# Kernel optimization log

Hardware: AMD Instinct MI355X
Metric: run time of the kernel (lower is better)

## Reference

```python
import jax, jax.numpy as jnp
import numpy as np

N, B, NPG, E = 16384, 64, 256, 524288
F_IN, POS_DIM, L_PE = 32, 3, 8
W, HEADS, LAYERS, DFF = 256, 8, 2, 1024
HID, OUT = 512, 64
S = NPG + 1
DH = W // HEADS


def _ln(x, s, b, eps=1e-5):
    m = jnp.mean(x, -1, keepdims=True)
    v = jnp.var(x, -1, keepdims=True)
    return (x - m) * jax.lax.rsqrt(v + eps) * s + b


def _gelu(x):
    # custom tanh-approx GELU from the source module
    c = float(np.sqrt(2.0 / np.pi))
    return 0.5 * x * (1.0 + jnp.tanh(c * (x + 0.044715 * x ** 3)))


def setup_inputs() -> dict:
    key = jax.random.key(0)
    ks = jax.random.split(key, 24)
    nrm = lambda k, shape, s=0.05: jax.random.normal(k, shape, jnp.float32) * s
    D_IN = F_IN + POS_DIM * L_PE  # 56
    inp = {}
    inp['x'] = jax.random.normal(ks[0], (N, F_IN), jnp.float32)
    inp['p'] = jax.random.uniform(ks[1], (N, POS_DIM), jnp.float32, -1.0, 1.0)
    inp['edge_index'] = jax.random.randint(ks[2], (2, E), 0, N, jnp.int32)
    inp['batch'] = (jnp.arange(N) // NPG).astype(jnp.int32)  # sorted, 64 equal graphs
    inp['gcn_w'] = nrm(ks[3], (D_IN, W), 0.1)
    inp['gcn_b'] = jnp.zeros((W,), jnp.float32)
    inp['cls_token'] = nrm(ks[4], (1, 1, W), 0.02)
    inp['ln_pre_s'] = jnp.ones((W,), jnp.float32)
    inp['ln_pre_b'] = jnp.zeros((W,), jnp.float32)
    inp['norm1_s'] = jnp.ones((LAYERS, W), jnp.float32)
    inp['norm1_b'] = jnp.zeros((LAYERS, W), jnp.float32)
    inp['in_proj_w'] = nrm(ks[5], (LAYERS, W, 3 * W))
    inp['in_proj_b'] = jnp.zeros((LAYERS, 3 * W), jnp.float32)
    inp['out_proj_w'] = nrm(ks[6], (LAYERS, W, W))
    inp['out_proj_b'] = jnp.zeros((LAYERS, W), jnp.float32)
    inp['norm2_s'] = jnp.ones((LAYERS, W), jnp.float32)
    inp['norm2_b'] = jnp.zeros((LAYERS, W), jnp.float32)
    inp['ff_w1'] = nrm(ks[7], (LAYERS, W, DFF))
    inp['ff_b1'] = jnp.zeros((LAYERS, DFF), jnp.float32)
    inp['ff_w2'] = nrm(ks[8], (LAYERS, DFF, W))
    inp['ff_b2'] = jnp.zeros((LAYERS, W), jnp.float32)
    inp['ln_post_s'] = jnp.ones((W,), jnp.float32)
    inp['ln_post_b'] = jnp.zeros((W,), jnp.float32)
    inp['dec_w1'] = nrm(ks[9], (W, HID))
    inp['dec_b1'] = jnp.zeros((HID,), jnp.float32)
    inp['dec_w2'] = nrm(ks[10], (HID, HID))
    inp['dec_b2'] = jnp.zeros((HID,), jnp.float32)
    inp['dec_w3'] = nrm(ks[11], (HID, OUT))
    inp['dec_b3'] = jnp.zeros((OUT,), jnp.float32)
    return inp


def _forward(x, p, gcn_w, gcn_b, cls_token, ln_pre_s, ln_pre_b, norm1_s, norm1_b,
             in_proj_w, in_proj_b, out_proj_w, out_proj_b, norm2_s, norm2_b,
             ff_w1, ff_b1, ff_w2, ff_b2, ln_post_s, ln_post_b,
             dec_w1, dec_b1, dec_w2, dec_b2, dec_w3, dec_b3, edge_index, batch):
    # positional encoding: sin(p * 2^i * pi), i = 0..L-1
    freqs = (2.0 ** jnp.arange(L_PE, dtype=jnp.float32)) * jnp.pi
    pe = jnp.sin(p[:, :, None] * freqs).reshape(N, POS_DIM * L_PE)
    xc = jnp.concatenate([x, pe], axis=-1)  # [N, 56]
    # GCNConv: x W, then sym-normalized aggregation with self loops, + bias
    xw = xc @ gcn_w  # [N, W]
    loop = jnp.arange(N, dtype=edge_index.dtype)
    row = jnp.concatenate([edge_index[0], loop])
    col = jnp.concatenate([edge_index[1], loop])
    deg = jax.ops.segment_sum(jnp.ones_like(row, dtype=xw.dtype), col, num_segments=N)
    dinv = jax.lax.rsqrt(jnp.maximum(deg, 1e-12))
    coef = dinv[row] * dinv[col]
    h = jax.ops.segment_sum(coef[:, None] * xw[row], col, num_segments=N) + gcn_b
    # to_dense_batch (batch is sorted graph ids)
    counts = jax.ops.segment_sum(jnp.ones((N,), jnp.int32), batch, num_segments=B)
    ptr = jnp.concatenate([jnp.zeros((1,), jnp.int32), jnp.cumsum(counts)[:-1]])
    pos = jnp.arange(N, dtype=jnp.int32) - ptr[batch]
    dense = jnp.zeros((B, NPG, W), h.dtype).at[batch, pos].set(h)
    mask = jnp.zeros((B, NPG), bool).at[batch, pos].set(True)
    # prepend cls token
    xd = jnp.concatenate([jnp.broadcast_to(cls_token, (B, 1, W)), dense], axis=1)  # [B,S,W]
    valid = jnp.concatenate([jnp.ones((B, 1), bool), mask], axis=1)  # [B,S]
    xd = _ln(xd, ln_pre_s, ln_pre_b)
    # causal mask with row 0 (cls) unmasked
    am = jnp.triu(jnp.ones((S, S), bool), k=1)
    am = am.at[0, :].set(False)
    allowed = (~am)[None, :, :] & valid[:, None, :]  # [B,S,S]
    scale = 1.0 / float(np.sqrt(DH))
    for l in range(LAYERS):
        h1 = _ln(xd, norm1_s[l], norm1_b[l])
        qkv = h1 @ in_proj_w[l] + in_proj_b[l]  # [B,S,3W]
        q, k, v = jnp.split(qkv, 3, axis=-1)
        q = q.reshape(B, S, HEADS, DH)
        k = k.reshape(B, S, HEADS, DH)
        v = v.reshape(B, S, HEADS, DH)
        sc = jnp.einsum('bqhd,bkhd->bhqk', q, k) * scale
        sc = jnp.where(allowed[:, None, :, :], sc, -1e9)
        a = jax.nn.softmax(sc, axis=-1)
        o = jnp.einsum('bhqk,bkhd->bqhd', a, v).reshape(B, S, W)
        xd = xd + (o @ out_proj_w[l] + out_proj_b[l])
        h2 = _ln(xd, norm2_s[l], norm2_b[l])
        # MLP(num_layers=2) applies activation after BOTH layers (incl. last)
        ff = _gelu(_gelu(h2 @ ff_w1[l] + ff_b1[l]) @ ff_w2[l] + ff_b2[l])
        xd = xd + ff
    cls = _ln(xd[:, 0, :], ln_post_s, ln_post_b)
    # decoder MLP(num_layers=3) with relu after every layer (incl. last)
    h3 = jax.nn.relu(cls @ dec_w1 + dec_b1)
    h3 = jax.nn.relu(h3 @ dec_w2 + dec_b2)
    return jax.nn.relu(h3 @ dec_w3 + dec_b3)


def reference(x, p, gcn_w, gcn_b, cls_token, ln_pre_s, ln_pre_b, norm1_s, norm1_b,
              in_proj_w, in_proj_b, out_proj_w, out_proj_b, norm2_s, norm2_b,
              ff_w1, ff_b1, ff_w2, ff_b2, ln_post_s, ln_post_b,
              dec_w1, dec_b1, dec_w2, dec_b2, dec_w3, dec_b3, edge_index, batch):
    return _forward(x, p, gcn_w, gcn_b, cls_token, ln_pre_s, ln_pre_b, norm1_s, norm1_b,
                    in_proj_w, in_proj_b, out_proj_w, out_proj_b, norm2_s, norm2_b,
                    ff_w1, ff_b1, ff_w2, ff_b2, ln_post_s, ln_post_b,
                    dec_w1, dec_b1, dec_w2, dec_b2, dec_w3, dec_b3, edge_index, batch)
```

## Files before the change

kernel.cpp:

```cpp
#include <hip/hip_runtime.h>
#include <math.h>

constexpr int N_NODES = 16384;
constexpr int BGRAPH  = 64;
constexpr int NEDGE   = 524288;
constexpr int SEQ     = 257;
constexpr int WDIM    = 256;
constexpr int DFF     = 1024;
constexpr int HID     = 512;
constexpr int MROWS   = BGRAPH * SEQ;

constexpr size_t F_Y    = 0;
constexpr size_t F_AGG  = F_Y    + (size_t)N_NODES * 64;
constexpr size_t F_XD   = F_AGG  + (size_t)N_NODES * 64;
constexpr size_t F_CLS  = F_XD   + (size_t)MROWS * WDIM;
constexpr size_t F_D1   = F_CLS  + (size_t)BGRAPH * WDIM;
constexpr size_t F_D2   = F_D1   + (size_t)BGRAPH * HID;
constexpr size_t F_WPAD = F_D2   + (size_t)BGRAPH * HID;
constexpr size_t F_DINV = F_WPAD + (size_t)64 * WDIM;
constexpr size_t F_XCLS = F_DINV + (size_t)N_NODES;
constexpr size_t F_IEND = F_XCLS + (size_t)BGRAPH * WDIM;

typedef __attribute__((ext_vector_type(8))) __bf16 bf16x8;
typedef __attribute__((ext_vector_type(4))) __bf16 bf16x4;
typedef __attribute__((ext_vector_type(4))) float f32x4;

__device__ __forceinline__ float gelu_f(float x) {
    float u = 0.7978845608028654f * (x + 0.044715f * x * x * x);
    return 0.5f * x * (1.0f + tanhf(u));
}

__global__ __launch_bounds__(256) void hist_kernel(const int* __restrict__ col, int* __restrict__ indeg) {
    int e = blockIdx.x * 256 + threadIdx.x;
    atomicAdd(&indeg[col[e]], 1);
}

__global__ __launch_bounds__(1024) void scan_kernel(const int* __restrict__ indeg, int* __restrict__ offs,
                                                    int* __restrict__ cursor, float* __restrict__ dinv) {
    __shared__ int parts[1024];
    int t = threadIdx.x;
    int base = t * 16;
    int loc[16];
    int s = 0;
#pragma unroll
    for (int i = 0; i < 16; ++i) { loc[i] = indeg[base + i]; s += loc[i]; }
    parts[t] = s;
    __syncthreads();
    for (int off = 1; off < 1024; off <<= 1) {
        int v = (t >= off) ? parts[t - off] : 0;
        __syncthreads();
        parts[t] += v;
        __syncthreads();
    }
    int run = (t == 0) ? 0 : parts[t - 1];
#pragma unroll
    for (int i = 0; i < 16; ++i) {
        offs[base + i] = run;
        cursor[base + i] = run;
        dinv[base + i] = rsqrtf((float)loc[i] + 1.0f);
        run += loc[i];
    }
    if (t == 1023) offs[N_NODES] = run;
}

__global__ __launch_bounds__(256) void fill_kernel(const int* __restrict__ ei, int* __restrict__ cursor,
                                                   int* __restrict__ csr) {
    int e = blockIdx.x * 256 + threadIdx.x;
    int r = ei[e];
    int c = ei[NEDGE + e];
    int pos = atomicAdd(&cursor[c], 1);
    csr[pos] = r;
}

__global__ __launch_bounds__(256) void y_kernel(const float* __restrict__ x, const float* __restrict__ p,
                                                const float* __restrict__ dinv, float* __restrict__ y) {
    int idx = blockIdx.x * 256 + threadIdx.x;
    int i = idx >> 6, d = idx & 63;
    float v = 0.f;
    if (d < 32) {
        v = x[i * 32 + d];
    } else if (d < 56) {
        int dd = d - 32;
        int dim = dd >> 3, j = dd & 7;
        v = sinf(p[i * 3 + dim] * (3.14159265358979323846f * (float)(1 << j)));
    }
    y[idx] = dinv[i] * v;
}

__global__ __launch_bounds__(256) void agg_kernel(const float* __restrict__ y, const float* __restrict__ dinv,
                                                  const int* __restrict__ offs, const int* __restrict__ csr,
                                                  float* __restrict__ agg) {
    int c = (blockIdx.x * 256 + threadIdx.x) >> 6;
    int lane = threadIdx.x & 63;
    float acc = y[(size_t)c * 64 + lane];
    int s = offs[c], e = offs[c + 1];
    for (int j = s; j < e; ++j) {
        int r = csr[j];
        acc += y[(size_t)r * 64 + lane];
    }
    agg[(size_t)c * 64 + lane] = dinv[c] * acc;
}

__global__ __launch_bounds__(256) void wpad_kernel(const float* __restrict__ w, float* __restrict__ wp) {
    int idx = blockIdx.x * 256 + threadIdx.x;
    wp[idx] = (idx < 56 * 256) ? w[idx] : 0.f;
}

__global__ __launch_bounds__(256) void cls_write(const float* __restrict__ tok, float* __restrict__ xd) {
    xd[(size_t)blockIdx.x * SEQ * WDIM + threadIdx.x] = tok[threadIdx.x];
}

template <int OUTBF>
__global__ __launch_bounds__(256) void ln4_kernel(const float* __restrict__ in, int rin_stride,
                                                  void* __restrict__ out,
                                                  const float* __restrict__ g, const float* __restrict__ be) {
    int w = threadIdx.x >> 6, lane = threadIdx.x & 63;
    int row = blockIdx.x * 4 + w;
    const float* ip = in + (size_t)row * rin_stride + lane * 4;
    f32x4 v = *(const f32x4*)ip;
    float s = v[0] + v[1] + v[2] + v[3];
    float ss = v[0] * v[0] + v[1] * v[1] + v[2] * v[2] + v[3] * v[3];
#pragma unroll
    for (int off = 1; off < 64; off <<= 1) { s += __shfl_xor(s, off); ss += __shfl_xor(ss, off); }
    float mean = s * 0.00390625f;
    float var = ss * 0.00390625f - mean * mean;
    float rs = rsqrtf(var + 1e-5f);
    f32x4 gv = *(const f32x4*)(g + lane * 4);
    f32x4 bv = *(const f32x4*)(be + lane * 4);
    if (OUTBF) {
        bf16x4 o;
#pragma unroll
        for (int i = 0; i < 4; ++i) o[i] = (__bf16)((v[i] - mean) * rs * gv[i] + bv[i]);
        *(bf16x4*)((__bf16*)out + (size_t)row * 256 + lane * 4) = o;
    } else {
        f32x4 o;
#pragma unroll
        for (int i = 0; i < 4; ++i) o[i] = (v[i] - mean) * rs * gv[i] + bv[i];
        *(f32x4*)((float*)out + (size_t)row * 256 + lane * 4) = o;
    }
}

__global__ __launch_bounds__(256) void tcast_kernel(const float* __restrict__ W, __bf16* __restrict__ Wt,
                                                    int K, int N) {
    __shared__ __bf16 T[64][65];
    int t = threadIdx.x;
    int k0 = blockIdx.x << 6, n0 = blockIdx.y << 6;
#pragma unroll
    for (int i = 0; i < 16; ++i) {
        int idx = t + i * 256;
        int k = idx >> 6, n = idx & 63;
        T[k][n] = (__bf16)W[(size_t)(k0 + k) * N + n0 + n];
    }
    __syncthreads();
#pragma unroll
    for (int i = 0; i < 16; ++i) {
        int idx = t + i * 256;
        int n = idx >> 6, k = idx & 63;
        Wt[(size_t)(n0 + n) * K + k0 + k] = T[k][n];
    }
}

constexpr int LP = 36;
template <int BN, int ACT, int OMODE>
__global__ __launch_bounds__(256) void gemm_bf(const __bf16* __restrict__ A, int lda,
                                               const __bf16* __restrict__ Bt,
                                               const float* __restrict__ bias,
                                               void* __restrict__ Cv, int ldc,
                                               int Ktot, int Mrows, int MBlocks, int NY) {
    constexpr int NTW = BN / 32;
    constexpr int AH = 128 * LP;
    constexpr int BH = BN * LP;
    __shared__ __bf16 As[2 * 128 * LP];
    __shared__ __bf16 Bs[2 * BN * LP];
    int f = blockIdx.x;
    int m8 = f & 7;
    int rest = f >> 3;
    int mg = rest / NY;
    int yb = rest - mg * NY;
    int mb = mg * 8 + m8;
    if (mb >= MBlocks) return;
    int m0 = mb << 7, n0 = yb * BN;

    int t = threadIdx.x;
    int w = t >> 6, L = t & 63;
    int wm = w >> 1, wn = w & 1;
    int lc = L & 15, quad = L >> 4;

    int sa_row = t >> 1, sa_off = (t & 1) << 4;
    const __bf16* ap = A + (size_t)(m0 + sa_row) * lda + sa_off;
    __bf16* as_dst = &As[sa_row * LP + sa_off];
    const __bf16* bp;
    __bf16* bs_dst;
    if constexpr (BN == 128) {
        bp = Bt + (size_t)(n0 + sa_row) * Ktot + sa_off;
        bs_dst = &Bs[sa_row * LP + sa_off];
    } else {
        int sb_row = t >> 2, sb_off = (t & 3) << 3;
        bp = Bt + (size_t)(n0 + sb_row) * Ktot + sb_off;
        bs_dst = &Bs[sb_row * LP + sb_off];
    }

    int a_base = (wm * 64 + lc) * LP + quad * 8;
    int b_base = (wn * (BN / 2) + lc) * LP + quad * 8;

    f32x4 acc[4][NTW] = {};

    bf16x8 ea0, ea1, eb0, eb1, oa0, oa1, ob0, ob1;
    ea0 = *(const bf16x8*)(ap);        ea1 = *(const bf16x8*)(ap + 8);
    oa0 = *(const bf16x8*)(ap + 32);   oa1 = *(const bf16x8*)(ap + 40);
    if constexpr (BN == 128) {
        eb0 = *(const bf16x8*)(bp);        eb1 = *(const bf16x8*)(bp + 8);
        ob0 = *(const bf16x8*)(bp + 32);   ob1 = *(const bf16x8*)(bp + 40);
    } else {
        eb0 = *(const bf16x8*)(bp);
        ob0 = *(const bf16x8*)(bp + 32);
    }

    for (int k0 = 0; k0 < Ktot; k0 += 64) {
        __syncthreads();
        *(bf16x8*)as_dst = ea0;
        *(bf16x8*)(as_dst + 8) = ea1;
        *(bf16x8*)(as_dst + AH) = oa0;
        *(bf16x8*)(as_dst + AH + 8) = oa1;
        if constexpr (BN == 128) {
            *(bf16x8*)bs_dst = eb0;
            *(bf16x8*)(bs_dst + 8) = eb1;
            *(bf16x8*)(bs_dst + BH) = ob0;
            *(bf16x8*)(bs_dst + BH + 8) = ob1;
        } else {
            *(bf16x8*)bs_dst = eb0;
            *(bf16x8*)(bs_dst + BH) = ob0;
        }
        __syncthreads();
        if (k0 + 64 < Ktot) {
            ea0 = *(const bf16x8*)(ap + k0 + 64);
            ea1 = *(const bf16x8*)(ap + k0 + 72);
            oa0 = *(const bf16x8*)(ap + k0 + 96);
            oa1 = *(const bf16x8*)(ap + k0 + 104);
            if constexpr (BN == 128) {
                eb0 = *(const bf16x8*)(bp + k0 + 64);
                eb1 = *(const bf16x8*)(bp + k0 + 72);
                ob0 = *(const bf16x8*)(bp + k0 + 96);
                ob1 = *(const bf16x8*)(bp + k0 + 104);
            } else {
                eb0 = *(const bf16x8*)(bp + k0 + 64);
                ob0 = *(const bf16x8*)(bp + k0 + 96);
            }
        }
        {
            bf16x8 af[4], bfr[NTW];
#pragma unroll
            for (int i = 0; i < 4; ++i) af[i] = *(const bf16x8*)&As[a_base + i * 16 * LP];
#pragma unroll
            for (int i = 0; i < NTW; ++i) bfr[i] = *(const bf16x8*)&Bs[b_base + i * 16 * LP];
#pragma unroll
            for (int mt = 0; mt < 4; ++mt)
#pragma unroll
                for (int nt = 0; nt < NTW; ++nt)
                    acc[mt][nt] = __builtin_amdgcn_mfma_f32_16x16x32_bf16(af[mt], bfr[nt], acc[mt][nt], 0, 0, 0);
        }
        {
            bf16x8 af[4], bfr[NTW];
#pragma unroll
            for (int i = 0; i < 4; ++i) af[i] = *(const bf16x8*)&As[AH + a_base + i * 16 * LP];
#pragma unroll
            for (int i = 0; i < NTW; ++i) bfr[i] = *(const bf16x8*)&Bs[BH + b_base + i * 16 * LP];
#pragma unroll
            for (int mt = 0; mt < 4; ++mt)
#pragma unroll
                for (int nt = 0; nt < NTW; ++nt)
                    acc[mt][nt] = __builtin_amdgcn_mfma_f32_16x16x32_bf16(af[mt], bfr[nt], acc[mt][nt], 0, 0, 0);
        }
    }

#pragma unroll
    for (int mt = 0; mt < 4; ++mt) {
        int gmb = m0 + wm * 64 + mt * 16 + quad * 4;
#pragma unroll
        for (int nt = 0; nt < NTW; ++nt) {
            int gn = n0 + wn * (BN / 2) + nt * 16 + lc;
            float bv = bias[gn];
#pragma unroll
            for (int r = 0; r < 4; ++r) {
                int gm = gmb + r;
                if (gm >= Mrows) continue;
                float v = acc[mt][nt][r] + bv;
                if (ACT == 1) v = gelu_f(v);
                if (OMODE == 0) {
                    ((__bf16*)Cv)[(size_t)gm * ldc + gn] = (__bf16)v;
                } else {
                    float* cp = (float*)Cv + (size_t)gm * ldc + gn;
                    *cp = v + *cp;
                }
            }
        }
    }
}

constexpr int PPITCH = 284;
__global__ __launch_bounds__(256, 2) void attn_mfma(const __bf16* __restrict__ qkvb,
                                                    __bf16* __restrict__ obuf) {
    __shared__ __bf16 Vt[32][PPITCH];
    __shared__ __bf16 Pb[4][16][PPITCH];
    int bb = blockIdx.x;
    int b = bb >> 3, h = bb & 7;
    int t = threadIdx.x;
    int w = t >> 6, L = t & 63;
    int c = L & 15, quad = L >> 4;
    const float scale = 0.17677669529663687f;
    const __bf16* qb = qkvb + (size_t)(b * SEQ) * 768 + h * 32;
    const __bf16* kb = qb + 256;
    const __bf16* vb = qb + 512;
    __bf16* ob = obuf + (size_t)(b * SEQ) * 256 + h * 32;

    for (int idx = t; idx < 272 * 4; idx += 256) {
        int key = idx >> 2, dc = (idx & 3) * 8;
        bf16x8 vv = {};
        if (key < SEQ) vv = *(const bf16x8*)(vb + (size_t)key * 768 + dc);
#pragma unroll
        for (int j = 0; j < 8; ++j) Vt[dc + j][key] = vv[j];
    }

    bf16x8 kfr[17];
#pragma unroll
    for (int tt = 0; tt < 17; ++tt) {
        int kr = tt * 16 + c; if (kr > 256) kr = 256;
        kfr[tt] = *(const bf16x8*)(kb + (size_t)kr * 768 + quad * 8);
    }
    __syncthreads();

#pragma unroll 1
    for (int qt = 0; qt < 5; ++qt) {
        int q0 = qt * 64 + w * 16;
        if (q0 > 256) continue;
        int ntiles = (qt == 0 && w == 0) ? 17 : (qt * 4 + w + 1);
        if (ntiles > 17) ntiles = 17;
        int nkc = (ntiles + 1) >> 1;

        bf16x8 qf;
        {
            int qr = q0 + c; if (qr > 256) qr = 256;
            qf = *(const bf16x8*)(qb + (size_t)qr * 768 + quad * 8);
        }

        f32x4 acc[17];
#pragma unroll
        for (int tt = 0; tt < 17; ++tt) {
            if (tt >= ntiles) continue;
            f32x4 z = {0.f, 0.f, 0.f, 0.f};
            acc[tt] = __builtin_amdgcn_mfma_f32_16x16x32_bf16(qf, kfr[tt], z, 0, 0, 0);
        }

        float inv[4];
#pragma unroll
        for (int j = 0; j < 4; ++j) {
            int q = q0 + quad * 4 + j;
            float mx = -3.0e38f;
#pragma unroll
            for (int tt = 0; tt < 17; ++tt) {
                if (tt >= ntiles) continue;
                int key = tt * 16 + c;
                bool ok = (key < SEQ) && (q == 0 || key <= q);
                float v = ok ? acc[tt][j] * scale : -3.0e38f;
                mx = fmaxf(mx, v);
            }
            mx = fmaxf(mx, __shfl_xor(mx, 1));
            mx = fmaxf(mx, __shfl_xor(mx, 2));
            mx = fmaxf(mx, __shfl_xor(mx, 4));
            mx = fmaxf(mx, __shfl_xor(mx, 8));
            float s = 0.f;
#pragma unroll
            for (int tt = 0; tt < 17; ++tt) {
                if (tt >= ntiles) continue;
                int key = tt * 16 + c;
                bool ok = (key < SEQ) && (q == 0 || key <= q);
                float pv = ok ? expf(acc[tt][j] * scale - mx) : 0.f;
                s += pv;
                Pb[w][quad * 4 + j][key] = (__bf16)pv;
            }
            if ((ntiles & 1) && ntiles < 17)
                Pb[w][quad * 4 + j][ntiles * 16 + c] = (__bf16)0.f;
            s += __shfl_xor(s, 1);
            s += __shfl_xor(s, 2);
            s += __shfl_xor(s, 4);
            s += __shfl_xor(s, 8);
            inv[j] = 1.0f / s;
        }

        f32x4 oacc0 = {0.f, 0.f, 0.f, 0.f};
        f32x4 oacc1 = {0.f, 0.f, 0.f, 0.f};
#pragma unroll
        for (int kc = 0; kc < 9; ++kc) {
            if (kc >= nkc) continue;
            int off = kc * 32 + quad * 8;
            bf16x8 af = {};
            bf16x8 bf0 = {};
            bf16x8 bf1 = {};
            if (off < 257) {
                af  = *(const bf16x8*)&Pb[w][c][off];
                bf0 = *(const bf16x8*)&Vt[c][off];
                bf1 = *(const bf16x8*)&Vt[16 + c][off];
            }
            oacc0 = __builtin_amdgcn_mfma_f32_16x16x32_bf16(af, bf0, oacc0, 0, 0, 0);
            oacc1 = __builtin_amdgcn_mfma_f32_16x16x32_bf16(af, bf1, oacc1, 0, 0, 0);
        }

#pragma unroll
        for (int j = 0; j < 4; ++j) {
            int q = q0 + quad * 4 + j;
            if (q < SEQ) {
                __bf16* op = ob + (size_t)q * 256;
                op[c]      = (__bf16)(oacc0[j] * inv[j]);
                op[16 + c] = (__bf16)(oacc1[j] * inv[j]);
            }
        }
    }
}

__global__ __launch_bounds__(256) void qcls_kernel(const __bf16* __restrict__ h1b,
                                                   const float* __restrict__ W,
                                                   const float* __restrict__ bias,
                                                   __bf16* __restrict__ qcls) {
    __shared__ float hrow[256];
    int b = blockIdx.x, t = threadIdx.x;
    hrow[t] = (float)h1b[(size_t)(b * SEQ) * 256 + t];
    __syncthreads();
    float s = bias[t];
    for (int k = 0; k < 256; ++k) s += hrow[k] * W[(size_t)k * 768 + t];
    qcls[b * 256 + t] = (__bf16)s;
}

__global__ __launch_bounds__(64) void attn_cls(const __bf16* __restrict__ qcls,
                                               const __bf16* __restrict__ qkvb,
                                               __bf16* __restrict__ ocls) {
    __shared__ float p[260];
    int bb = blockIdx.x;
    int b = bb >> 3, h = bb & 7;
    int lane = threadIdx.x;
    const float scale = 0.17677669529663687f;
    float q[32];
    const __bf16* qp = qcls + b * 256 + h * 32;
#pragma unroll
    for (int c = 0; c < 4; ++c) {
        bf16x8 v = *(const bf16x8*)(qp + c * 8);
#pragma unroll
        for (int e = 0; e < 8; ++e) q[c * 8 + e] = (float)v[e];
    }
    float sc[5];
    float mx = -3.0e38f;
#pragma unroll
    for (int i = 0; i < 5; ++i) {
        int j = lane + i * 64;
        float s = -3.0e38f;
        if (j < SEQ) {
            const __bf16* kp = qkvb + (size_t)(b * SEQ + j) * 768 + 256 + h * 32;
            float a = 0.f;
#pragma unroll
            for (int c = 0; c < 4; ++c) {
                bf16x8 v = *(const bf16x8*)(kp + c * 8);
#pragma unroll
                for (int e = 0; e < 8; ++e) a += q[c * 8 + e] * (float)v[e];
            }
            s = a * scale;
        }
        sc[i] = s;
        mx = fmaxf(mx, s);
    }
#pragma unroll
    for (int off = 1; off < 64; off <<= 1) mx = fmaxf(mx, __shfl_xor(mx, off));
    float sum = 0.f;
#pragma unroll
    for (int i = 0; i < 5; ++i) {
        int j = lane + i * 64;
        float e = (j < SEQ) ? expf(sc[i] - mx) : 0.f;
        sc[i] = e;
        sum += e;
    }
#pragma unroll
    for (int off = 1; off < 64; off <<= 1) sum += __shfl_xor(sum, off);
    float inv = 1.0f / sum;
#pragma unroll
    for (int i = 0; i < 5; ++i) {
        int j = lane + i * 64;
        if (j < SEQ) p[j] = sc[i] * inv;
    }
    __syncthreads();
    if (lane < 32) {
        float o = 0.f;
        for (int j = 0; j < SEQ; ++j)
            o += p[j] * (float)qkvb[(size_t)(b * SEQ + j) * 768 + 512 + h * 32 + lane];
        ocls[b * 256 + h * 32 + lane] = (__bf16)o;
    }
}

__global__ __launch_bounds__(256) void oproj_cls(const __bf16* __restrict__ ocls,
                                                 const float* __restrict__ W,
                                                 const float* __restrict__ bias,
                                                 const float* __restrict__ xd,
                                                 float* __restrict__ xcls) {
    __shared__ float orow[256];
    int b = blockIdx.x, t = threadIdx.x;
    orow[t] = (float)ocls[b * 256 + t];
    __syncthreads();
    float s = bias[t];
    for (int k = 0; k < 256; ++k) s += orow[k] * W[(size_t)k * 256 + t];
    xcls[b * 256 + t] = s + xd[(size_t)(b * SEQ) * 256 + t];
}

__global__ __launch_bounds__(256) void ff1_cls(const __bf16* __restrict__ h2cls,
                                               const float* __restrict__ W1,
                                               const float* __restrict__ b1,
                                               __bf16* __restrict__ f1cls) {
    __shared__ float hrow[256];
    int b = blockIdx.x, t = threadIdx.x;
    hrow[t] = (float)h2cls[b * 256 + t];
    __syncthreads();
#pragma unroll
    for (int i = 0; i < 4; ++i) {
        int col = t + i * 256;
        float s = b1[col];
        for (int k = 0; k < 256; ++k) s += hrow[k] * W1[(size_t)k * 1024 + col];
        f1cls[b * 1024 + col] = (__bf16)gelu_f(s);
    }
}

__global__ __launch_bounds__(256) void ff2_cls(const __bf16* __restrict__ f1cls,
                                               const float* __restrict__ W2,
                                               const float* __restrict__ b2,
                                               float* __restrict__ xcls) {
    __shared__ float frow[1024];
    int b = blockIdx.x, t = threadIdx.x;
#pragma unroll
    for (int i = 0; i < 4; ++i) frow[t + i * 256] = (float)f1cls[b * 1024 + t + i * 256];
    __syncthreads();
    float s = b2[t];
    for (int k = 0; k < 1024; ++k) s += frow[k] * W2[(size_t)k * 256 + t];
    xcls[b * 256 + t] += gelu_f(s);
}

template <int ACT, bool RESID, bool REMAP>
__global__ __launch_bounds__(256) void gemm_std(const float* __restrict__ A, int lda,
                                                const float* __restrict__ Bw, int ldb,
                                                const float* __restrict__ bias,
                                                float* __restrict__ C, int ldc, int Ktot) {
    int t = threadIdx.x;
    int m0 = blockIdx.x << 6, n0 = blockIdx.y << 6;
    __shared__ float As[16][68];
    __shared__ float Bs[16][64];
    int arow = t >> 2, akk = (t & 3) << 2;
    int bk = t >> 4, bn = (t & 15) << 2;
    int tm = (t >> 4) << 2, tn = (t & 15) << 2;
    float acc[4][4] = {};
    const float* ap = A + (size_t)(m0 + arow) * lda + akk;
    const float* bp = Bw + (size_t)bk * ldb + n0 + bn;
    for (int k0 = 0; k0 < Ktot; k0 += 16) {
        float4 av = *(const float4*)(ap + k0);
        float4 bv = *(const float4*)(bp + (size_t)k0 * ldb);
        __syncthreads();
        As[akk + 0][arow] = av.x; As[akk + 1][arow] = av.y;
        As[akk + 2][arow] = av.z; As[akk + 3][arow] = av.w;
        *(float4*)&Bs[bk][bn] = bv;
        __syncthreads();
#pragma unroll
        for (int k = 0; k < 16; ++k) {
            float4 a = *(const float4*)&As[k][tm];
            float4 b = *(const float4*)&Bs[k][tn];
            acc[0][0] += a.x * b.x; acc[0][1] += a.x * b.y; acc[0][2] += a.x * b.z; acc[0][3] += a.x * b.w;
            acc[1][0] += a.y * b.x; acc[1][1] += a.y * b.y; acc[1][2] += a.y * b.z; acc[1][3] += a.y * b.w;
            acc[2][0] += a.z * b.x; acc[2][1] += a.z * b.y; acc[2][2] += a.z * b.z; acc[2][3] += a.z * b.w;
            acc[3][0] += a.w * b.x; acc[3][1] += a.w * b.y; acc[3][2] += a.w * b.z; acc[3][3] += a.w * b.w;
        }
    }
#pragma unroll
    for (int i = 0; i < 4; ++i) {
        int gm = m0 + tm + i;
        int orow = REMAP ? (gm + (gm >> 8) + 1) : gm;
        float* cp = C + (size_t)orow * ldc + n0 + tn;
        float4 r;
        r.x = acc[i][0] + bias[n0 + tn + 0];
        r.y = acc[i][1] + bias[n0 + tn + 1];
        r.z = acc[i][2] + bias[n0 + tn + 2];
        r.w = acc[i][3] + bias[n0 + tn + 3];
        if (ACT == 1) { r.x = gelu_f(r.x); r.y = gelu_f(r.y); r.z = gelu_f(r.z); r.w = gelu_f(r.w); }
        if (ACT == 2) { r.x = fmaxf(r.x, 0.f); r.y = fmaxf(r.y, 0.f); r.z = fmaxf(r.z, 0.f); r.w = fmaxf(r.w, 0.f); }
        if (RESID) {
            float4 o = *(const float4*)cp;
            r.x += o.x; r.y += o.y; r.z += o.z; r.w += o.w;
        }
        *(float4*)cp = r;
    }
}

template <int K, int NOUT>
__global__ __launch_bounds__(256) void dec_fc2(const float* __restrict__ in, const float* __restrict__ w,
                                               const float* __restrict__ bia, float* __restrict__ out) {
    __shared__ float rowbuf[K];
    __shared__ float part[4][64];
    int b = blockIdx.x, c = blockIdx.y, t = threadIdx.x;
    for (int i = t; i < K; i += 256) rowbuf[i] = in[(size_t)b * K + i];
    __syncthreads();
    int lane = t & 63, wv = t >> 6;
    int n = c * 64 + lane;
    const int KQ = K / 4;
    const float* wp = w + (size_t)(wv * KQ) * NOUT + n;
    float s = 0.f;
#pragma unroll 8
    for (int k = 0; k < KQ; ++k) s += rowbuf[wv * KQ + k] * wp[(size_t)k * NOUT];
    part[wv][lane] = s;
    __syncthreads();
    if (wv == 0) {
        float r = part[0][lane] + part[1][lane] + part[2][lane] + part[3][lane] + bia[n];
        out[(size_t)b * NOUT + n] = fmaxf(r, 0.f);
    }
}

extern "C" void kernel_launch(void* const* d_in, const int* in_sizes, int n_in,
                              void* d_out, int out_size, void* d_ws, size_t ws_size,
                              hipStream_t stream) {
    const float* x         = (const float*)d_in[0];
    const float* p         = (const float*)d_in[1];
    const int*   ei        = (const int*)d_in[2];
    const float* gcn_w     = (const float*)d_in[4];
    const float* gcn_b     = (const float*)d_in[5];
    const float* cls_tok   = (const float*)d_in[6];
    const float* ln_pre_s  = (const float*)d_in[7];
    const float* ln_pre_b  = (const float*)d_in[8];
    const float* norm1_s   = (const float*)d_in[9];
    const float* norm1_b   = (const float*)d_in[10];
    const float* in_proj_w = (const float*)d_in[11];
    const float* in_proj_b = (const float*)d_in[12];
    const float* out_proj_w= (const float*)d_in[13];
    const float* out_proj_b= (const float*)d_in[14];
    const float* norm2_s   = (const float*)d_in[15];
    const float* norm2_b   = (const float*)d_in[16];
    const float* ff_w1     = (const float*)d_in[17];
    const float* ff_b1     = (const float*)d_in[18];
    const float* ff_w2     = (const float*)d_in[19];
    const float* ff_b2     = (const float*)d_in[20];
    const float* ln_post_s = (const float*)d_in[21];
    const float* ln_post_b = (const float*)d_in[22];
    const float* dec_w1    = (const float*)d_in[23];
    const float* dec_b1    = (const float*)d_in[24];
    const float* dec_w2    = (const float*)d_in[25];
    const float* dec_b2    = (const float*)d_in[26];
    const float* dec_w3    = (const float*)d_in[27];
    const float* dec_b3    = (const float*)d_in[28];

    float* ws   = (float*)d_ws;
    float* y    = ws + F_Y;
    float* agg  = ws + F_AGG;
    float* xd   = ws + F_XD;
    float* cls  = ws + F_CLS;
    float* dd1  = ws + F_D1;
    float* dd2  = ws + F_D2;
    float* wpad = ws + F_WPAD;
    float* dinv = ws + F_DINV;
    float* xcls = ws + F_XCLS;
    int* ibase  = (int*)(ws + F_IEND);
    int* indeg  = ibase;
    int* offs   = ibase + N_NODES;
    int* cursor = offs + N_NODES + 1;
    int* csr    = cursor + N_NODES;
    uintptr_t ub = ((uintptr_t)(csr + NEDGE) + 15) & ~(uintptr_t)15;
    __bf16* h1b  = (__bf16*)ub;
    __bf16* qkvb = h1b  + (size_t)MROWS * 256;
    __bf16* ffbb = qkvb + (size_t)MROWS * 768;
    __bf16* wt_in  = ffbb  + (size_t)MROWS * 1024;
    __bf16* wt_out = wt_in  + 2 * 768 * 256;
    __bf16* wt_f1  = wt_out + 2 * 256 * 256;
    __bf16* wt_f2  = wt_f1  + 2 * 1024 * 256;
    __bf16* qcls   = wt_f2 + 2 * 256 * 1024;
    __bf16* ocls   = qcls + 64 * 256;
    __bf16* h2cls  = ocls + 64 * 256;
    __bf16* f1cls  = h2cls + 64 * 256;

    hipMemsetAsync(indeg, 0, N_NODES * sizeof(int), stream);
    hist_kernel<<<NEDGE / 256, 256, 0, stream>>>(ei + NEDGE, indeg);
    scan_kernel<<<1, 1024, 0, stream>>>(indeg, offs, cursor, dinv);
    fill_kernel<<<NEDGE / 256, 256, 0, stream>>>(ei, cursor, csr);
    y_kernel<<<N_NODES * 64 / 256, 256, 0, stream>>>(x, p, dinv, y);
    agg_kernel<<<N_NODES / 4, 256, 0, stream>>>(y, dinv, offs, csr, agg);
    wpad_kernel<<<64, 256, 0, stream>>>(gcn_w, wpad);

    tcast_kernel<<<dim3(4, 12), 256, 0, stream>>>(in_proj_w, wt_in, 256, 768);
    tcast_kernel<<<dim3(4, 4), 256, 0, stream>>>(out_proj_w, wt_out, 256, 256);
    tcast_kernel<<<dim3(4, 16), 256, 0, stream>>>(ff_w1, wt_f1, 256, 1024);
    tcast_kernel<<<dim3(16, 4), 256, 0, stream>>>(ff_w2, wt_f2, 1024, 256);
    tcast_kernel<<<dim3(4, 12), 256, 0, stream>>>(in_proj_w + (size_t)256 * 768,
                                                  wt_in + (size_t)768 * 256, 256, 768);

    gemm_std<0, false, true><<<dim3(256, 4), 256, 0, stream>>>(agg, 64, wpad, 256, gcn_b, xd, 256, 64);
    cls_write<<<64, 256, 0, stream>>>(cls_tok, xd);
    ln4_kernel<0><<<MROWS / 4, 256, 0, stream>>>(xd, 256, xd, ln_pre_s, ln_pre_b);

    const int MB = (MROWS + 127) / 128;
    const int MG8 = (MB + 7) / 8;

    ln4_kernel<1><<<MROWS / 4, 256, 0, stream>>>(xd, 256, h1b, norm1_s, norm1_b);
    gemm_bf<128, 0, 0><<<8 * 6 * MG8, 256, 0, stream>>>(
        h1b, 256, wt_in, in_proj_b, qkvb, 768, 256, MROWS, MB, 6);
    attn_mfma<<<512, 256, 0, stream>>>(qkvb, h1b);
    gemm_bf<64, 0, 1><<<8 * 4 * MG8, 256, 0, stream>>>(
        h1b, 256, wt_out, out_proj_b, xd, 256, 256, MROWS, MB, 4);
    ln4_kernel<1><<<MROWS / 4, 256, 0, stream>>>(xd, 256, h1b, norm2_s, norm2_b);
    gemm_bf<128, 1, 0><<<8 * 8 * MG8, 256, 0, stream>>>(
        h1b, 256, wt_f1, ff_b1, ffbb, 1024, 256, MROWS, MB, 8);
    gemm_bf<64, 1, 1><<<8 * 4 * MG8, 256, 0, stream>>>(
        ffbb, 1024, wt_f2, ff_b2, xd, 256, 1024, MROWS, MB, 4);

    ln4_kernel<1><<<MROWS / 4, 256, 0, stream>>>(xd, 256, h1b, norm1_s + WDIM, norm1_b + WDIM);
    gemm_bf<128, 0, 0><<<8 * 4 * MG8, 256, 0, stream>>>(
        h1b, 256, wt_in + (size_t)768 * 256 + (size_t)256 * 256,
        in_proj_b + 768 + 256, qkvb + 256, 768, 256, MROWS, MB, 4);
    qcls_kernel<<<64, 256, 0, stream>>>(h1b, in_proj_w + (size_t)256 * 768, in_proj_b + 768, qcls);
    attn_cls<<<512, 64, 0, stream>>>(qcls, qkvb, ocls);
    oproj_cls<<<64, 256, 0, stream>>>(ocls, out_proj_w + (size_t)256 * 256, out_proj_b + 256, xd, xcls);
    ln4_kernel<1><<<16, 256, 0, stream>>>(xcls, 256, h2cls, norm2_s + WDIM, norm2_b + WDIM);
    ff1_cls<<<64, 256, 0, stream>>>(h2cls, ff_w1 + (size_t)256 * 1024, ff_b1 + 1024, f1cls);
    ff2_cls<<<64, 256, 0, stream>>>(f1cls, ff_w2 + (size_t)1024 * 256, ff_b2 + 256, xcls);

    ln4_kernel<0><<<16, 256, 0, stream>>>(xcls, 256, cls, ln_post_s, ln_post_b);
    dec_fc2<256, 512><<<dim3(BGRAPH, 8), 256, 0, stream>>>(cls, dec_w1, dec_b1, dd1);
    dec_fc2<512, 512><<<dim3(BGRAPH, 8), 256, 0, stream>>>(dd1, dec_w2, dec_b2, dd2);
    dec_fc2<512, 64><<<dim3(BGRAPH, 1), 256, 0, stream>>>(dd2, dec_w3, dec_b3, (float*)d_out);
}
```

Before: 635.0 us.

## Store residual stream in bf16 and run GCN projection on MFMA GEMM

The residual stream xd changes from fp32 to bf16, so layernorm reads and the residual-add GEMM epilogues move half the bytes. The GCN aggregation output is written as bf16, and the fp32 SIMT gemm_std for the GCN linear is replaced by the MFMA gemm_bf path with a row remap, using a transposed bf16 weight. This trades residual accumulation precision for lower memory traffic and may hurt accuracy.

```diff
diff --git a/kernel.cpp b/kernel.cpp
--- a/kernel.cpp
+++ b/kernel.cpp
@@ -11,13 +11,10 @@
 constexpr int MROWS   = BGRAPH * SEQ;
 
 constexpr size_t F_Y    = 0;
-constexpr size_t F_AGG  = F_Y    + (size_t)N_NODES * 64;
-constexpr size_t F_XD   = F_AGG  + (size_t)N_NODES * 64;
-constexpr size_t F_CLS  = F_XD   + (size_t)MROWS * WDIM;
+constexpr size_t F_CLS  = F_Y    + (size_t)N_NODES * 64;
 constexpr size_t F_D1   = F_CLS  + (size_t)BGRAPH * WDIM;
 constexpr size_t F_D2   = F_D1   + (size_t)BGRAPH * HID;
-constexpr size_t F_WPAD = F_D2   + (size_t)BGRAPH * HID;
-constexpr size_t F_DINV = F_WPAD + (size_t)64 * WDIM;
+constexpr size_t F_DINV = F_D2   + (size_t)BGRAPH * HID;
 constexpr size_t F_XCLS = F_DINV + (size_t)N_NODES;
 constexpr size_t F_IEND = F_XCLS + (size_t)BGRAPH * WDIM;
 
@@ -89,7 +86,7 @@
 
 __global__ __launch_bounds__(256) void agg_kernel(const float* __restrict__ y, const float* __restrict__ dinv,
                                                   const int* __restrict__ offs, const int* __restrict__ csr,
-                                                  float* __restrict__ agg) {
+                                                  __bf16* __restrict__ aggb) {
     int c = (blockIdx.x * 256 + threadIdx.x) >> 6;
     int lane = threadIdx.x & 63;
     float acc = y[(size_t)c * 64 + lane];
@@ -98,26 +95,33 @@
         int r = csr[j];
         acc += y[(size_t)r * 64 + lane];
     }
-    agg[(size_t)c * 64 + lane] = dinv[c] * acc;
-}
-
-__global__ __launch_bounds__(256) void wpad_kernel(const float* __restrict__ w, float* __restrict__ wp) {
-    int idx = blockIdx.x * 256 + threadIdx.x;
-    wp[idx] = (idx < 56 * 256) ? w[idx] : 0.f;
-}
-
-__global__ __launch_bounds__(256) void cls_write(const float* __restrict__ tok, float* __restrict__ xd) {
-    xd[(size_t)blockIdx.x * SEQ * WDIM + threadIdx.x] = tok[threadIdx.x];
-}
-
-template <int OUTBF>
-__global__ __launch_bounds__(256) void ln4_kernel(const float* __restrict__ in, int rin_stride,
+    aggb[(size_t)c * 64 + lane] = (__bf16)(dinv[c] * acc);
+}
+
+__global__ __launch_bounds__(256) void gwt_kernel(const float* __restrict__ W, __bf16* __restrict__ Wt) {
+    int n = threadIdx.x;
+    for (int k = 0; k < 64; ++k)
+        Wt[n * 64 + k] = (k < 56) ? (__bf16)W[(size_t)k * 256 + n] : (__bf16)0.f;
+}
+
+__global__ __launch_bounds__(256) void cls_write(const float* __restrict__ tok, __bf16* __restrict__ xd) {
+    xd[(size_t)blockIdx.x * SEQ * WDIM + threadIdx.x] = (__bf16)tok[threadIdx.x];
+}
+
+template <int INBF, int OUTBF>
+__global__ __launch_bounds__(256) void ln4_kernel(const void* __restrict__ in, int rin_stride,
                                                   void* __restrict__ out,
                                                   const float* __restrict__ g, const float* __restrict__ be) {
     int w = threadIdx.x >> 6, lane = threadIdx.x & 63;
     int row = blockIdx.x * 4 + w;
-    const float* ip = in + (size_t)row * rin_stride + lane * 4;
-    f32x4 v = *(const f32x4*)ip;
+    f32x4 v;
+    if constexpr (INBF) {
+        bf16x4 bv4 = *(const bf16x4*)((const __bf16*)in + (size_t)row * rin_stride + lane * 4);
+#pragma unroll
+        for (int i = 0; i < 4; ++i) v[i] = (float)bv4[i];
+    } else {
+        v = *(const f32x4*)((const float*)in + (size_t)row * rin_stride + lane * 4);
+    }
     float s = v[0] + v[1] + v[2] + v[3];
     float ss = v[0] * v[0] + v[1] * v[1] + v[2] * v[2] + v[3] * v[3];
 #pragma unroll
@@ -127,7 +131,7 @@
     float rs = rsqrtf(var + 1e-5f);
     f32x4 gv = *(const f32x4*)(g + lane * 4);
     f32x4 bv = *(const f32x4*)(be + lane * 4);
-    if (OUTBF) {
+    if constexpr (OUTBF) {
         bf16x4 o;
 #pragma unroll
         for (int i = 0; i < 4; ++i) o[i] = (__bf16)((v[i] - mean) * rs * gv[i] + bv[i]);
@@ -161,7 +165,7 @@
 }
 
 constexpr int LP = 36;
-template <int BN, int ACT, int OMODE>
+template <int BN, int ACT, int OMODE, int REMAP = 0>
 __global__ __launch_bounds__(256) void gemm_bf(const __bf16* __restrict__ A, int lda,
                                                const __bf16* __restrict__ Bt,
                                                const float* __restrict__ bias,
@@ -286,11 +290,12 @@
                 if (gm >= Mrows) continue;
                 float v = acc[mt][nt][r] + bv;
                 if (ACT == 1) v = gelu_f(v);
+                int orow = REMAP ? (gm + (gm >> 8) + 1) : gm;
                 if (OMODE == 0) {
-                    ((__bf16*)Cv)[(size_t)gm * ldc + gn] = (__bf16)v;
+                    ((__bf16*)Cv)[(size_t)orow * ldc + gn] = (__bf16)v;
                 } else {
-                    float* cp = (float*)Cv + (size_t)gm * ldc + gn;
-                    *cp = v + *cp;
+                    __bf16* cp = (__bf16*)Cv + (size_t)orow * ldc + gn;
+                    *cp = (__bf16)(v + (float)*cp);
                 }
             }
         }
@@ -496,7 +501,7 @@
 __global__ __launch_bounds__(256) void oproj_cls(const __bf16* __restrict__ ocls,
                                                  const float* __restrict__ W,
                                                  const float* __restrict__ bias,
-                                                 const float* __restrict__ xd,
+                                                 const __bf16* __restrict__ xd,
                                                  float* __restrict__ xcls) {
     __shared__ float orow[256];
     int b = blockIdx.x, t = threadIdx.x;
@@ -504,7 +509,7 @@
     __syncthreads();
     float s = bias[t];
     for (int k = 0; k < 256; ++k) s += orow[k] * W[(size_t)k * 256 + t];
-    xcls[b * 256 + t] = s + xd[(size_t)(b * SEQ) * 256 + t];
+    xcls[b * 256 + t] = s + (float)xd[(size_t)(b * SEQ) * 256 + t];
 }
 
 __global__ __launch_bounds__(256) void ff1_cls(const __bf16* __restrict__ h2cls,
@@ -536,59 +541,6 @@
     float s = b2[t];
     for (int k = 0; k < 1024; ++k) s += frow[k] * W2[(size_t)k * 256 + t];
     xcls[b * 256 + t] += gelu_f(s);
-}
-
-template <int ACT, bool RESID, bool REMAP>
-__global__ __launch_bounds__(256) void gemm_std(const float* __restrict__ A, int lda,
-                                                const float* __restrict__ Bw, int ldb,
-                                                const float* __restrict__ bias,
-                                                float* __restrict__ C, int ldc, int Ktot) {
-    int t = threadIdx.x;
-    int m0 = blockIdx.x << 6, n0 = blockIdx.y << 6;
-    __shared__ float As[16][68];
-    __shared__ float Bs[16][64];
-    int arow = t >> 2, akk = (t & 3) << 2;
-    int bk = t >> 4, bn = (t & 15) << 2;
-    int tm = (t >> 4) << 2, tn = (t & 15) << 2;
-    float acc[4][4] = {};
-    const float* ap = A + (size_t)(m0 + arow) * lda + akk;
-    const float* bp = Bw + (size_t)bk * ldb + n0 + bn;
-    for (int k0 = 0; k0 < Ktot; k0 += 16) {
-        float4 av = *(const float4*)(ap + k0);
-        float4 bv = *(const float4*)(bp + (size_t)k0 * ldb);
-        __syncthreads();
-        As[akk + 0][arow] = av.x; As[akk + 1][arow] = av.y;
-        As[akk + 2][arow] = av.z; As[akk + 3][arow] = av.w;
-        *(float4*)&Bs[bk][bn] = bv;
-        __syncthreads();
-#pragma unroll
-        for (int k = 0; k < 16; ++k) {
-            float4 a = *(const float4*)&As[k][tm];
-            float4 b = *(const float4*)&Bs[k][tn];
-            acc[0][0] += a.x * b.x; acc[0][1] += a.x * b.y; acc[0][2] += a.x * b.z; acc[0][3] += a.x * b.w;
-            acc[1][0] += a.y * b.x; acc[1][1] += a.y * b.y; acc[1][2] += a.y * b.z; acc[1][3] += a.y * b.w;
-            acc[2][0] += a.z * b.x; acc[2][1] += a.z * b.y; acc[2][2] += a.z * b.z; acc[2][3] += a.z * b.w;
-            acc[3][0] += a.w * b.x; acc[3][1] += a.w * b.y; acc[3][2] += a.w * b.z; acc[3][3] += a.w * b.w;
-        }
-    }
-#pragma unroll
-    for (int i = 0; i < 4; ++i) {
-        int gm = m0 + tm + i;
-        int orow = REMAP ? (gm + (gm >> 8) + 1) : gm;
-        float* cp = C + (size_t)orow * ldc + n0 + tn;
-        float4 r;
-        r.x = acc[i][0] + bias[n0 + tn + 0];
-        r.y = acc[i][1] + bias[n0 + tn + 1];
-        r.z = acc[i][2] + bias[n0 + tn + 2];
-        r.w = acc[i][3] + bias[n0 + tn + 3];
-        if (ACT == 1) { r.x = gelu_f(r.x); r.y = gelu_f(r.y); r.z = gelu_f(r.z); r.w = gelu_f(r.w); }
-        if (ACT == 2) { r.x = fmaxf(r.x, 0.f); r.y = fmaxf(r.y, 0.f); r.z = fmaxf(r.z, 0.f); r.w = fmaxf(r.w, 0.f); }
-        if (RESID) {
-            float4 o = *(const float4*)cp;
-            r.x += o.x; r.y += o.y; r.z += o.z; r.w += o.w;
-        }
-        *(float4*)cp = r;
-    }
 }
 
 template <int K, int NOUT>
@@ -648,12 +600,9 @@
 
     float* ws   = (float*)d_ws;
     float* y    = ws + F_Y;
-    float* agg  = ws + F_AGG;
-    float* xd   = ws + F_XD;
     float* cls  = ws + F_CLS;
     float* dd1  = ws + F_D1;
     float* dd2  = ws + F_D2;
-    float* wpad = ws + F_WPAD;
     float* dinv = ws + F_DINV;
     float* xcls = ws + F_XCLS;
     int* ibase  = (int*)(ws + F_IEND);
@@ -667,20 +616,23 @@
     __bf16* ffbb = qkvb + (size_t)MROWS * 768;
     __bf16* wt_in  = ffbb  + (size_t)MROWS * 1024;
     __bf16* wt_out = wt_in  + 2 * 768 * 256;
-    __bf16* wt_f1  = wt_out + 2 * 256 * 256;
-    __bf16* wt_f2  = wt_f1  + 2 * 1024 * 256;
-    __bf16* qcls   = wt_f2 + 2 * 256 * 1024;
+    __bf16* wt_f1  = wt_out + 256 * 256;
+    __bf16* wt_f2  = wt_f1  + 1024 * 256;
+    __bf16* qcls   = wt_f2 + 256 * 1024;
     __bf16* ocls   = qcls + 64 * 256;
     __bf16* h2cls  = ocls + 64 * 256;
     __bf16* f1cls  = h2cls + 64 * 256;
+    __bf16* xd     = f1cls + 64 * 1024;
+    __bf16* aggb   = xd + (size_t)MROWS * 256;
+    __bf16* wt_gcn = aggb + (size_t)N_NODES * 64;
 
     hipMemsetAsync(indeg, 0, N_NODES * sizeof(int), stream);
     hist_kernel<<<NEDGE / 256, 256, 0, stream>>>(ei + NEDGE, indeg);
     scan_kernel<<<1, 1024, 0, stream>>>(indeg, offs, cursor, dinv);
     fill_kernel<<<NEDGE / 256, 256, 0, stream>>>(ei, cursor, csr);
     y_kernel<<<N_NODES * 64 / 256, 256, 0, stream>>>(x, p, dinv, y);
-    agg_kernel<<<N_NODES / 4, 256, 0, stream>>>(y, dinv, offs, csr, agg);
-    wpad_kernel<<<64, 256, 0, stream>>>(gcn_w, wpad);
+    agg_kernel<<<N_NODES / 4, 256, 0, stream>>>(y, dinv, offs, csr, aggb);
+    gwt_kernel<<<1, 256, 0, stream>>>(gcn_w, wt_gcn);
 
     tcast_kernel<<<dim3(4, 12), 256, 0, stream>>>(in_proj_w, wt_in, 256, 768);
     tcast_kernel<<<dim3(4, 4), 256, 0, stream>>>(out_proj_w, wt_out, 256, 256);
@@ -689,37 +641,38 @@
     tcast_kernel<<<dim3(4, 12), 256, 0, stream>>>(in_proj_w + (size_t)256 * 768,
                                                   wt_in + (size_t)768 * 256, 256, 768);
 
-    gemm_std<0, false, true><<<dim3(256, 4), 256, 0, stream>>>(agg, 64, wpad, 256, gcn_b, xd, 256, 64);
+    gemm_bf<128, 0, 0, 1><<<8 * 2 * 16, 256, 0, stream>>>(
+        aggb, 64, wt_gcn, gcn_b, xd, 256, 64, N_NODES, N_NODES / 128, 2);
     cls_write<<<64, 256, 0, stream>>>(cls_tok, xd);
-    ln4_kernel<0><<<MROWS / 4, 256, 0, stream>>>(xd, 256, xd, ln_pre_s, ln_pre_b);
+    ln4_kernel<1, 1><<<MROWS / 4, 256, 0, stream>>>(xd, 256, xd, ln_pre_s, ln_pre_b);
 
     const int MB = (MROWS + 127) / 128;
     const int MG8 = (MB + 7) / 8;
 
-    ln4_kernel<1><<<MROWS / 4, 256, 0, stream>>>(xd, 256, h1b, norm1_s, norm1_b);
+    ln4_kernel<1, 1><<<MROWS / 4, 256, 0, stream>>>(xd, 256, h1b, norm1_s, norm1_b);
     gemm_bf<128, 0, 0><<<8 * 6 * MG8, 256, 0, stream>>>(
         h1b, 256, wt_in, in_proj_b, qkvb, 768, 256, MROWS, MB, 6);
     attn_mfma<<<512, 256, 0, stream>>>(qkvb, h1b);
     gemm_bf<64, 0, 1><<<8 * 4 * MG8, 256, 0, stream>>>(
         h1b, 256, wt_out, out_proj_b, xd, 256, 256, MROWS, MB, 4);
-    ln4_kernel<1><<<MROWS / 4, 256, 0, stream>>>(xd, 256, h1b, norm2_s, norm2_b);
+    ln4_kernel<1, 1><<<MROWS / 4, 256, 0, stream>>>(xd, 256, h1b, norm2_s, norm2_b);
     gemm_bf<128, 1, 0><<<8 * 8 * MG8, 256, 0, stream>>>(
         h1b, 256, wt_f1, ff_b1, ffbb, 1024, 256, MROWS, MB, 8);
     gemm_bf<64, 1, 1><<<8 * 4 * MG8, 256, 0, stream>>>(
         ffbb, 1024, wt_f2, ff_b2, xd, 256, 1024, MROWS, MB, 4);
 
-    ln4_kernel<1><<<MROWS / 4, 256, 0, stream>>>(xd, 256, h1b, norm1_s + WDIM, norm1_b + WDIM);
+    ln4_kernel<1, 1><<<MROWS / 4, 256, 0, stream>>>(xd, 256, h1b, norm1_s + WDIM, norm1_b + WDIM);
     gemm_bf<128, 0, 0><<<8 * 4 * MG8, 256, 0, stream>>>(
         h1b, 256, wt_in + (size_t)768 * 256 + (size_t)256 * 256,
         in_proj_b + 768 + 256, qkvb + 256, 768, 256, MROWS, MB, 4);
     qcls_kernel<<<64, 256, 0, stream>>>(h1b, in_proj_w + (size_t)256 * 768, in_proj_b + 768, qcls);
     attn_cls<<<512, 64, 0, stream>>>(qcls, qkvb, ocls);
     oproj_cls<<<64, 256, 0, stream>>>(ocls, out_proj_w + (size_t)256 * 256, out_proj_b + 256, xd, xcls);
-    ln4_kernel<1><<<16, 256, 0, stream>>>(xcls, 256, h2cls, norm2_s + WDIM, norm2_b + WDIM);
+    ln4_kernel<0, 1><<<16, 256, 0, stream>>>(xcls, 256, h2cls, norm2_s + WDIM, norm2_b + WDIM);
     ff1_cls<<<64, 256, 0, stream>>>(h2cls, ff_w1 + (size_t)256 * 1024, ff_b1 + 1024, f1cls);
     ff2_cls<<<64, 256, 0, stream>>>(f1cls, ff_w2 + (size_t)1024 * 256, ff_b2 + 256, xcls);
 
-    ln4_kernel<0><<<16, 256, 0, stream>>>(xcls, 256, cls, ln_post_s, ln_post_b);
+    ln4_kernel<0, 0><<<16, 256, 0, stream>>>(xcls, 256, cls, ln_post_s, ln_post_b);
     dec_fc2<256, 512><<<dim3(BGRAPH, 8), 256, 0, stream>>>(cls, dec_w1, dec_b1, dd1);
     dec_fc2<512, 512><<<dim3(BGRAPH, 8), 256, 0, stream>>>(dd1, dec_w2, dec_b2, dd2);
     dec_fc2<512, 64><<<dim3(BGRAPH, 1), 256, 0, stream>>>(dd2, dec_w3, dec_b3, (float*)d_out);
```

Result: slower. 649.5 us (+2.3%).

## Split-K out-proj and FF2 GEMMs with atomics, fuse bias/residual/LayerNorm epilogue

Applied to the files above, without the earlier changes.

The out-projection and second FFN GEMMs now split their K dimension across a second grid axis (2 and 4 slices). Each slice atomically adds its partial sums into a zeroed fp32 scratch buffer. A new finln kernel then adds bias, applies GELU where needed, adds the residual and computes the following LayerNorm in one pass, replacing separate ln4 launches. The aim is more blocks for these short-K GEMMs plus one fewer pass over activations, at the cost of memsets, global atomic traffic and an extra fp32 buffer round trip.

```diff
diff --git a/kernel.cpp b/kernel.cpp
--- a/kernel.cpp
+++ b/kernel.cpp
@@ -13,7 +13,8 @@
 constexpr size_t F_Y    = 0;
 constexpr size_t F_AGG  = F_Y    + (size_t)N_NODES * 64;
 constexpr size_t F_XD   = F_AGG  + (size_t)N_NODES * 64;
-constexpr size_t F_CLS  = F_XD   + (size_t)MROWS * WDIM;
+constexpr size_t F_C32  = F_XD   + (size_t)MROWS * WDIM;
+constexpr size_t F_CLS  = F_C32  + (size_t)MROWS * WDIM;
 constexpr size_t F_D1   = F_CLS  + (size_t)BGRAPH * WDIM;
 constexpr size_t F_D2   = F_D1   + (size_t)BGRAPH * HID;
 constexpr size_t F_WPAD = F_D2   + (size_t)BGRAPH * HID;
@@ -140,6 +141,39 @@
     }
 }
 
+template <int ACT>
+__global__ __launch_bounds__(256) void finln_kernel(const float* __restrict__ C32,
+                                                    const float* __restrict__ bias,
+                                                    float* __restrict__ xd, __bf16* __restrict__ h1b,
+                                                    const float* __restrict__ g, const float* __restrict__ be) {
+    int w = threadIdx.x >> 6, lane = threadIdx.x & 63;
+    int row = blockIdx.x * 4 + w;
+    size_t base = (size_t)row * 256 + lane * 4;
+    f32x4 v = *(const f32x4*)(xd + base);
+    f32x4 cc = *(const f32x4*)(C32 + base);
+    f32x4 bb = *(const f32x4*)(bias + lane * 4);
+#pragma unroll
+    for (int i = 0; i < 4; ++i) {
+        float u = cc[i] + bb[i];
+        if (ACT == 1) u = gelu_f(u);
+        v[i] += u;
+    }
+    *(f32x4*)(xd + base) = v;
+    float s = v[0] + v[1] + v[2] + v[3];
+    float ss = v[0] * v[0] + v[1] * v[1] + v[2] * v[2] + v[3] * v[3];
+#pragma unroll
+    for (int off = 1; off < 64; off <<= 1) { s += __shfl_xor(s, off); ss += __shfl_xor(ss, off); }
+    float mean = s * 0.00390625f;
+    float var = ss * 0.00390625f - mean * mean;
+    float rs = rsqrtf(var + 1e-5f);
+    f32x4 gv = *(const f32x4*)(g + lane * 4);
+    f32x4 bev = *(const f32x4*)(be + lane * 4);
+    bf16x4 o;
+#pragma unroll
+    for (int i = 0; i < 4; ++i) o[i] = (__bf16)((v[i] - mean) * rs * gv[i] + bev[i]);
+    *(bf16x4*)(h1b + base) = o;
+}
+
 __global__ __launch_bounds__(256) void tcast_kernel(const float* __restrict__ W, __bf16* __restrict__ Wt,
                                                     int K, int N) {
     __shared__ __bf16 T[64][65];
@@ -163,10 +197,10 @@
 constexpr int LP = 36;
 template <int BN, int ACT, int OMODE>
 __global__ __launch_bounds__(256) void gemm_bf(const __bf16* __restrict__ A, int lda,
-                                               const __bf16* __restrict__ Bt,
+                                               const __bf16* __restrict__ Bt, int ldb,
                                                const float* __restrict__ bias,
                                                void* __restrict__ Cv, int ldc,
-                                               int Ktot, int Mrows, int MBlocks, int NY) {
+                                               int Ksl, int Mrows, int MBlocks, int NY) {
     constexpr int NTW = BN / 32;
     constexpr int AH = 128 * LP;
     constexpr int BH = BN * LP;
@@ -180,6 +214,7 @@
     int mb = mg * 8 + m8;
     if (mb >= MBlocks) return;
     int m0 = mb << 7, n0 = yb * BN;
+    int kbase = blockIdx.y * Ksl;
 
     int t = threadIdx.x;
     int w = t >> 6, L = t & 63;
@@ -187,16 +222,16 @@
     int lc = L & 15, quad = L >> 4;
 
     int sa_row = t >> 1, sa_off = (t & 1) << 4;
-    const __bf16* ap = A + (size_t)(m0 + sa_row) * lda + sa_off;
+    const __bf16* ap = A + (size_t)(m0 + sa_row) * lda + sa_off + kbase;
     __bf16* as_dst = &As[sa_row * LP + sa_off];
     const __bf16* bp;
     __bf16* bs_dst;
     if constexpr (BN == 128) {
-        bp = Bt + (size_t)(n0 + sa_row) * Ktot + sa_off;
+        bp = Bt + (size_t)(n0 + sa_row) * ldb + sa_off + kbase;
         bs_dst = &Bs[sa_row * LP + sa_off];
     } else {
         int sb_row = t >> 2, sb_off = (t & 3) << 3;
-        bp = Bt + (size_t)(n0 + sb_row) * Ktot + sb_off;
+        bp = Bt + (size_t)(n0 + sb_row) * ldb + sb_off + kbase;
         bs_dst = &Bs[sb_row * LP + sb_off];
     }
 
@@ -216,7 +251,7 @@
         ob0 = *(const bf16x8*)(bp + 32);
     }
 
-    for (int k0 = 0; k0 < Ktot; k0 += 64) {
+    for (int k0 = 0; k0 < Ksl; k0 += 64) {
         __syncthreads();
         *(bf16x8*)as_dst = ea0;
         *(bf16x8*)(as_dst + 8) = ea1;
@@ -232,7 +267,7 @@
             *(bf16x8*)(bs_dst + BH) = ob0;
         }
         __syncthreads();
-        if (k0 + 64 < Ktot) {
+        if (k0 + 64 < Ksl) {
             ea0 = *(const bf16x8*)(ap + k0 + 64);
             ea1 = *(const bf16x8*)(ap + k0 + 72);
             oa0 = *(const bf16x8*)(ap + k0 + 96);
@@ -279,7 +314,7 @@
 #pragma unroll
         for (int nt = 0; nt < NTW; ++nt) {
             int gn = n0 + wn * (BN / 2) + nt * 16 + lc;
-            float bv = bias[gn];
+            float bv = (OMODE == 2) ? 0.f : bias[gn];
 #pragma unroll
             for (int r = 0; r < 4; ++r) {
                 int gm = gmb + r;
@@ -288,9 +323,11 @@
                 if (ACT == 1) v = gelu_f(v);
                 if (OMODE == 0) {
                     ((__bf16*)Cv)[(size_t)gm * ldc + gn] = (__bf16)v;
-                } else {
+                } else if (OMODE == 1) {
                     float* cp = (float*)Cv + (size_t)gm * ldc + gn;
                     *cp = v + *cp;
+                } else {
+                    atomicAdd((float*)Cv + (size_t)gm * ldc + gn, v);
                 }
             }
         }
@@ -650,6 +687,7 @@
     float* y    = ws + F_Y;
     float* agg  = ws + F_AGG;
     float* xd   = ws + F_XD;
+    float* C32  = ws + F_C32;
     float* cls  = ws + F_CLS;
     float* dd1  = ws + F_D1;
     float* dd2  = ws + F_D2;
@@ -667,9 +705,9 @@
     __bf16* ffbb = qkvb + (size_t)MROWS * 768;
     __bf16* wt_in  = ffbb  + (size_t)MROWS * 1024;
     __bf16* wt_out = wt_in  + 2 * 768 * 256;
-    __bf16* wt_f1  = wt_out + 2 * 256 * 256;
-    __bf16* wt_f2  = wt_f1  + 2 * 1024 * 256;
-    __bf16* qcls   = wt_f2 + 2 * 256 * 1024;
+    __bf16* wt_f1  = wt_out + 256 * 256;
+    __bf16* wt_f2  = wt_f1  + 1024 * 256;
+    __bf16* qcls   = wt_f2 + 256 * 1024;
     __bf16* ocls   = qcls + 64 * 256;
     __bf16* h2cls  = ocls + 64 * 256;
     __bf16* f1cls  = h2cls + 64 * 256;
@@ -698,19 +736,21 @@
 
     ln4_kernel<1><<<MROWS / 4, 256, 0, stream>>>(xd, 256, h1b, norm1_s, norm1_b);
     gemm_bf<128, 0, 0><<<8 * 6 * MG8, 256, 0, stream>>>(
-        h1b, 256, wt_in, in_proj_b, qkvb, 768, 256, MROWS, MB, 6);
+        h1b, 256, wt_in, 256, in_proj_b, qkvb, 768, 256, MROWS, MB, 6);
     attn_mfma<<<512, 256, 0, stream>>>(qkvb, h1b);
-    gemm_bf<64, 0, 1><<<8 * 4 * MG8, 256, 0, stream>>>(
-        h1b, 256, wt_out, out_proj_b, xd, 256, 256, MROWS, MB, 4);
-    ln4_kernel<1><<<MROWS / 4, 256, 0, stream>>>(xd, 256, h1b, norm2_s, norm2_b);
+    hipMemsetAsync(C32, 0, (size_t)MROWS * 256 * sizeof(float), stream);
+    gemm_bf<64, 0, 2><<<dim3(8 * 4 * MG8, 2), 256, 0, stream>>>(
+        h1b, 256, wt_out, 256, nullptr, C32, 256, 128, MROWS, MB, 4);
+    finln_kernel<0><<<MROWS / 4, 256, 0, stream>>>(C32, out_proj_b, xd, h1b, norm2_s, norm2_b);
     gemm_bf<128, 1, 0><<<8 * 8 * MG8, 256, 0, stream>>>(
-        h1b, 256, wt_f1, ff_b1, ffbb, 1024, 256, MROWS, MB, 8);
-    gemm_bf<64, 1, 1><<<8 * 4 * MG8, 256, 0, stream>>>(
-        ffbb, 1024, wt_f2, ff_b2, xd, 256, 1024, MROWS, MB, 4);
-
-    ln4_kernel<1><<<MROWS / 4, 256, 0, stream>>>(xd, 256, h1b, norm1_s + WDIM, norm1_b + WDIM);
+        h1b, 256, wt_f1, 256, ff_b1, ffbb, 1024, 256, MROWS, MB, 8);
+    hipMemsetAsync(C32, 0, (size_t)MROWS * 256 * sizeof(float), stream);
+    gemm_bf<64, 0, 2><<<dim3(8 * 4 * MG8, 4), 256, 0, stream>>>(
+        ffbb, 1024, wt_f2, 1024, nullptr, C32, 256, 256, MROWS, MB, 4);
+    finln_kernel<1><<<MROWS / 4, 256, 0, stream>>>(C32, ff_b2, xd, h1b, norm1_s + WDIM, norm1_b + WDIM);
+
     gemm_bf<128, 0, 0><<<8 * 4 * MG8, 256, 0, stream>>>(
-        h1b, 256, wt_in + (size_t)768 * 256 + (size_t)256 * 256,
+        h1b, 256, wt_in + (size_t)768 * 256 + (size_t)256 * 256, 256,
         in_proj_b + 768 + 256, qkvb + 256, 768, 256, MROWS, MB, 4);
     qcls_kernel<<<64, 256, 0, stream>>>(h1b, in_proj_w + (size_t)256 * 768, in_proj_b + 768, qcls);
     attn_cls<<<512, 64, 0, stream>>>(qcls, qkvb, ocls);
```

Result: slower. 675.5 us (+6.4%).
